# Performance work log

Hardware: AMD Instinct MI355X
Metric: run time of the kernel (lower is better)

The kernel has to match this reference:

```python
import jax, jax.numpy as jnp
import numpy as np

BN_EPS = 1e-5

def setup_inputs() -> dict:
    key = jax.random.key(0)
    ks = jax.random.split(key, 7)
    B, D, A = 16384, 768, 51
    s = 1.0 / np.sqrt(D)
    return {
        "x": jax.random.normal(ks[0], (B, D), dtype=jnp.float32),
        "W_embed": jax.random.uniform(ks[1], (D, D), minval=-s, maxval=s, dtype=jnp.float32),
        "b_embed": jax.random.uniform(ks[2], (D,), minval=-s, maxval=s, dtype=jnp.float32),
        "W_attr": jax.random.uniform(ks[3], (A, D), minval=-s, maxval=s, dtype=jnp.float32),  # stacked per-attribute (dim->1) heads
        "b_attr": jax.random.uniform(ks[4], (A,), minval=-s, maxval=s, dtype=jnp.float32),
        "gamma": jnp.ones((A,), dtype=jnp.float32),
        "beta": jnp.zeros((A,), dtype=jnp.float32),
    }

def reference(x, W_embed, b_embed, W_attr, b_attr, gamma, beta):
    # word_embed: Linear(dim, dim)
    h = x @ W_embed.T + b_embed                      # [B, D]
    # fused per-attribute heads: cat of attr_num (dim->1) linears == one (dim->attr_num) matmul
    logits = h @ W_attr.T + b_attr                    # [B, A]
    # BatchNorm1d (training mode: batch statistics, biased variance)
    mean = jnp.mean(logits, axis=0)
    var = jnp.var(logits, axis=0)
    y = (logits - mean) * jax.lax.rsqrt(var + BN_EPS) * gamma + beta
    return y
```

## Files before the change

kernel.cpp:

```cpp
#include <hip/hip_runtime.h>
#include <hip/hip_bf16.h>

typedef _Float16 halfx8 __attribute__((ext_vector_type(8)));
typedef _Float16 halfx4 __attribute__((ext_vector_type(4)));
typedef float floatx4 __attribute__((ext_vector_type(4)));

#define GLOBAL_AS __attribute__((address_space(1)))
#define LDS_AS __attribute__((address_space(3)))

__device__ __forceinline__ void async_copy_16(const _Float16* g, _Float16* l) {
    __builtin_amdgcn_global_load_lds((GLOBAL_AS void*)g, (LDS_AS void*)l, 16, 0, 0);
}

#define PM 16384
#define PD 768
#define PA 51
#define PA_PAD 64

__global__ void convert_x_kernel(const float* __restrict__ src, _Float16* __restrict__ dst) {
    int idx = blockIdx.x * 256 + threadIdx.x;
    float4 v = ((const float4*)src)[idx];
    halfx4 h;
    h[0] = (_Float16)v.x; h[1] = (_Float16)v.y; h[2] = (_Float16)v.z; h[3] = (_Float16)v.w;
    *(halfx4*)(dst + (size_t)idx * 4) = h;
}

__global__ void convert_w_kernel(const float* __restrict__ We, const float* __restrict__ Wa,
                                 _Float16* __restrict__ we16, _Float16* __restrict__ wa16,
                                 float* __restrict__ stats) {
    int b = blockIdx.x, t = threadIdx.x;
    if (b < 576) {
        int idx = b * 256 + t;
        float4 v = ((const float4*)We)[idx];
        halfx4 h;
        h[0] = (_Float16)v.x; h[1] = (_Float16)v.y; h[2] = (_Float16)v.z; h[3] = (_Float16)v.w;
        *(halfx4*)(we16 + (size_t)idx * 4) = h;
    } else if (b < 624) {
        int j = (b - 576) * 256 + t;
        halfx4 h;
        if (j < (PA * PD) / 4) {
            float4 v = ((const float4*)Wa)[j];
            h[0] = (_Float16)v.x; h[1] = (_Float16)v.y; h[2] = (_Float16)v.z; h[3] = (_Float16)v.w;
        } else {
            h[0] = (_Float16)0.f; h[1] = (_Float16)0.f; h[2] = (_Float16)0.f; h[3] = (_Float16)0.f;
        }
        *(halfx4*)(wa16 + (size_t)j * 4) = h;
    } else {
        if (t < 128) stats[t] = 0.f;
    }
}

__global__ __launch_bounds__(256) void gemm1_kernel(
    const _Float16* __restrict__ A,
    const _Float16* __restrict__ B,
    const float* __restrict__ bias,
    _Float16* __restrict__ H)
{
    __shared__ _Float16 As[128 * 64];
    __shared__ _Float16 Bs[128 * 64];
    const int tid = threadIdx.x;
    const int wave = tid >> 6;
    const int lane = tid & 63;
    const int quad = lane >> 4;
    const int l16 = lane & 15;
    const int wm = wave >> 1;
    const int wn = wave & 1;

    int b = blockIdx.x;
    int xcd = b & 7;
    int q = b >> 3;
    int mt = xcd * 16 + (q & 15);
    int nt = q >> 4;
    const int row0 = mt * 128;
    const int col0 = nt * 128;

    const int r_in = lane >> 3;
    const int koff = (lane & 7) * 8;

    const _Float16* Ag = A + (size_t)row0 * PD + koff;
    const _Float16* Bg = B + (size_t)col0 * PD + koff;

    floatx4 acc[4][4];
    #pragma unroll
    for (int i = 0; i < 4; ++i)
        #pragma unroll
        for (int j = 0; j < 4; ++j)
            acc[i][j] = (floatx4){0.f, 0.f, 0.f, 0.f};

    for (int kt = 0; kt < PD; kt += 64) {
        #pragma unroll
        for (int j = 0; j < 4; ++j) {
            int i = wave * 4 + j;
            async_copy_16(Ag + (size_t)(i * 8 + r_in) * PD + kt, &As[i * 512]);
            async_copy_16(Bg + (size_t)(i * 8 + r_in) * PD + kt, &Bs[i * 512]);
        }
        __syncthreads();
        #pragma unroll
        for (int ks = 0; ks < 2; ++ks) {
            halfx8 af[4], bf[4];
            #pragma unroll
            for (int mi = 0; mi < 4; ++mi)
                af[mi] = *(const halfx8*)&As[(wm * 64 + mi * 16 + l16) * 64 + ks * 32 + quad * 8];
            #pragma unroll
            for (int ni = 0; ni < 4; ++ni)
                bf[ni] = *(const halfx8*)&Bs[(wn * 64 + ni * 16 + l16) * 64 + ks * 32 + quad * 8];
            #pragma unroll
            for (int mi = 0; mi < 4; ++mi)
                #pragma unroll
                for (int ni = 0; ni < 4; ++ni)
                    acc[mi][ni] = __builtin_amdgcn_mfma_f32_16x16x32_f16(af[mi], bf[ni], acc[mi][ni], 0, 0, 0);
        }
        __syncthreads();
    }

    #pragma unroll
    for (int ni = 0; ni < 4; ++ni) {
        int col = col0 + wn * 64 + ni * 16 + l16;
        float bv = bias[col];
        #pragma unroll
        for (int mi = 0; mi < 4; ++mi) {
            int rowb = row0 + wm * 64 + mi * 16 + quad * 4;
            #pragma unroll
            for (int r = 0; r < 4; ++r)
                H[(size_t)(rowb + r) * PD + col] = (_Float16)(acc[mi][ni][r] + bv);
        }
    }
}

__global__ __launch_bounds__(256) void gemm2_kernel(
    const _Float16* __restrict__ Hm,
    const _Float16* __restrict__ Wa,
    const float* __restrict__ b_attr,
    float* __restrict__ logits,
    float* __restrict__ stats)
{
    __shared__ _Float16 As[128 * 64];
    __shared__ _Float16 Bs[64 * 64];
    __shared__ float s_sum[64];
    __shared__ float s_ssq[64];
    const int tid = threadIdx.x;
    const int wave = tid >> 6;
    const int lane = tid & 63;
    const int quad = lane >> 4;
    const int l16 = lane & 15;
    const int row0 = blockIdx.x * 128;
    const int r_in = lane >> 3;
    const int koff = (lane & 7) * 8;

    if (tid < 64) { s_sum[tid] = 0.f; s_ssq[tid] = 0.f; }

    const _Float16* Ag = Hm + (size_t)row0 * PD + koff;
    const _Float16* Bg = Wa + koff;

    floatx4 acc[2][4];
    #pragma unroll
    for (int i = 0; i < 2; ++i)
        #pragma unroll
        for (int j = 0; j < 4; ++j)
            acc[i][j] = (floatx4){0.f, 0.f, 0.f, 0.f};

    for (int kt = 0; kt < PD; kt += 64) {
        #pragma unroll
        for (int j = 0; j < 4; ++j) {
            int i = wave * 4 + j;
            async_copy_16(Ag + (size_t)(i * 8 + r_in) * PD + kt, &As[i * 512]);
        }
        #pragma unroll
        for (int j = 0; j < 2; ++j) {
            int i = wave * 2 + j;
            async_copy_16(Bg + (size_t)(i * 8 + r_in) * PD + kt, &Bs[i * 512]);
        }
        __syncthreads();
        #pragma unroll
        for (int ks = 0; ks < 2; ++ks) {
            halfx8 af[2], bf[4];
            #pragma unroll
            for (int mi = 0; mi < 2; ++mi)
                af[mi] = *(const halfx8*)&As[(wave * 32 + mi * 16 + l16) * 64 + ks * 32 + quad * 8];
            #pragma unroll
            for (int ni = 0; ni < 4; ++ni)
                bf[ni] = *(const halfx8*)&Bs[(ni * 16 + l16) * 64 + ks * 32 + quad * 8];
            #pragma unroll
            for (int mi = 0; mi < 2; ++mi)
                #pragma unroll
                for (int ni = 0; ni < 4; ++ni)
                    acc[mi][ni] = __builtin_amdgcn_mfma_f32_16x16x32_f16(af[mi], bf[ni], acc[mi][ni], 0, 0, 0);
        }
        __syncthreads();
    }

    #pragma unroll
    for (int ni = 0; ni < 4; ++ni) {
        int col = ni * 16 + l16;
        if (col < PA) {
            float bv = b_attr[col];
            float ps = 0.f, pss = 0.f;
            #pragma unroll
            for (int mi = 0; mi < 2; ++mi) {
                int rowb = row0 + wave * 32 + mi * 16 + quad * 4;
                #pragma unroll
                for (int r = 0; r < 4; ++r) {
                    float v = acc[mi][ni][r] + bv;
                    logits[(size_t)(rowb + r) * PA + col] = v;
                    ps += v; pss += v * v;
                }
            }
            atomicAdd(&s_sum[col], ps);
            atomicAdd(&s_ssq[col], pss);
        }
    }
    __syncthreads();
    if (tid < PA) {
        atomicAdd(&stats[tid], s_sum[tid]);
        atomicAdd(&stats[64 + tid], s_ssq[tid]);
    }
}

__global__ void bn_finalize_kernel(const float* __restrict__ logits,
                                   const float* __restrict__ stats,
                                   const float* __restrict__ gamma,
                                   const float* __restrict__ beta,
                                   float* __restrict__ out, int total) {
    __shared__ float s_scale[PA];
    __shared__ float s_shift[PA];
    int t = threadIdx.x;
    if (t < PA) {
        const float invB = 1.0f / (float)PM;
        float mean = stats[t] * invB;
        float var = stats[64 + t] * invB - mean * mean;
        float inv = rsqrtf(var + 1e-5f);
        float g = gamma[t] * inv;
        s_scale[t] = g;
        s_shift[t] = beta[t] - mean * g;
    }
    __syncthreads();
    int idx = blockIdx.x * 256 + t;
    if (idx < total) {
        int col = idx % PA;
        out[idx] = logits[idx] * s_scale[col] + s_shift[col];
    }
}

extern "C" void kernel_launch(void* const* d_in, const int* in_sizes, int n_in,
                              void* d_out, int out_size, void* d_ws, size_t ws_size,
                              hipStream_t stream) {
    const float* x       = (const float*)d_in[0];
    const float* W_embed = (const float*)d_in[1];
    const float* b_embed = (const float*)d_in[2];
    const float* W_attr  = (const float*)d_in[3];
    const float* b_attr  = (const float*)d_in[4];
    const float* gamma   = (const float*)d_in[5];
    const float* beta    = (const float*)d_in[6];
    float* out = (float*)d_out;

    char* ws = (char*)d_ws;
    _Float16* x_f16  = (_Float16*)(ws);
    _Float16* we16   = (_Float16*)(ws + 25165824);
    _Float16* wa16   = (_Float16*)(ws + 26345472);
    _Float16* h_f16  = (_Float16*)(ws + 26443776);
    float*    logits = (float*)   (ws + 51609600);
    float*    stats  = (float*)   (ws + 54951936);

    convert_x_kernel<<<12288, 256, 0, stream>>>(x, x_f16);
    convert_w_kernel<<<625, 256, 0, stream>>>(W_embed, W_attr, we16, wa16, stats);
    gemm1_kernel<<<768, 256, 0, stream>>>(x_f16, we16, b_embed, h_f16);
    gemm2_kernel<<<128, 256, 0, stream>>>(h_f16, wa16, b_attr, logits, stats);
    bn_finalize_kernel<<<3264, 256, 0, stream>>>(logits, stats, gamma, beta, out, PM * PA);
}
```

Before: 163.3 us.

## XOR-swizzle LDS layout, merge convert kernels, halve gemm2 row tile

Applies an XOR swizzle to the K-chunk index when staging A/B tiles into LDS in both GEMMs, so that the halfx8 fragment reads avoid LDS bank conflicts. Merges the x and weight fp16 conversion kernels into a single launch to save one kernel launch. Shrinks gemm2 tiles from 128 to 64 rows, doubling its grid to 256 blocks so more CUs are used, at the cost of more global stats atomics and less reuse of the Wa tile.

Result: faster. 153.3 us (-6.1%).

```diff
diff --git a/kernel.cpp b/kernel.cpp
--- a/kernel.cpp
+++ b/kernel.cpp
@@ -17,26 +17,26 @@
 #define PA 51
 #define PA_PAD 64
 
-__global__ void convert_x_kernel(const float* __restrict__ src, _Float16* __restrict__ dst) {
-    int idx = blockIdx.x * 256 + threadIdx.x;
-    float4 v = ((const float4*)src)[idx];
-    halfx4 h;
-    h[0] = (_Float16)v.x; h[1] = (_Float16)v.y; h[2] = (_Float16)v.z; h[3] = (_Float16)v.w;
-    *(halfx4*)(dst + (size_t)idx * 4) = h;
-}
-
-__global__ void convert_w_kernel(const float* __restrict__ We, const float* __restrict__ Wa,
-                                 _Float16* __restrict__ we16, _Float16* __restrict__ wa16,
-                                 float* __restrict__ stats) {
+
+__global__ void convert_all_kernel(const float* __restrict__ x, const float* __restrict__ We,
+                                   const float* __restrict__ Wa,
+                                   _Float16* __restrict__ x16, _Float16* __restrict__ we16,
+                                   _Float16* __restrict__ wa16, float* __restrict__ stats) {
     int b = blockIdx.x, t = threadIdx.x;
-    if (b < 576) {
+    if (b < 12288) {
         int idx = b * 256 + t;
+        float4 v = ((const float4*)x)[idx];
+        halfx4 h;
+        h[0] = (_Float16)v.x; h[1] = (_Float16)v.y; h[2] = (_Float16)v.z; h[3] = (_Float16)v.w;
+        *(halfx4*)(x16 + (size_t)idx * 4) = h;
+    } else if (b < 12288 + 576) {
+        int idx = (b - 12288) * 256 + t;
         float4 v = ((const float4*)We)[idx];
         halfx4 h;
         h[0] = (_Float16)v.x; h[1] = (_Float16)v.y; h[2] = (_Float16)v.z; h[3] = (_Float16)v.w;
         *(halfx4*)(we16 + (size_t)idx * 4) = h;
-    } else if (b < 624) {
-        int j = (b - 576) * 256 + t;
+    } else if (b < 12288 + 624) {
+        int j = (b - 12288 - 576) * 256 + t;
         halfx4 h;
         if (j < (PA * PD) / 4) {
             float4 v = ((const float4*)Wa)[j];
@@ -75,10 +75,10 @@
     const int col0 = nt * 128;
 
     const int r_in = lane >> 3;
-    const int koff = (lane & 7) * 8;
-
-    const _Float16* Ag = A + (size_t)row0 * PD + koff;
-    const _Float16* Bg = B + (size_t)col0 * PD + koff;
+    const int ksw = ((lane & 7) ^ r_in) * 8;
+
+    const _Float16* Ag = A + (size_t)row0 * PD + ksw;
+    const _Float16* Bg = B + (size_t)col0 * PD + ksw;
 
     floatx4 acc[4][4];
     #pragma unroll
@@ -100,10 +100,12 @@
             halfx8 af[4], bf[4];
             #pragma unroll
             for (int mi = 0; mi < 4; ++mi)
-                af[mi] = *(const halfx8*)&As[(wm * 64 + mi * 16 + l16) * 64 + ks * 32 + quad * 8];
+                af[mi] = *(const halfx8*)&As[(wm * 64 + mi * 16 + l16) * 64 +
+                                             (((ks * 4 + quad) ^ (l16 & 7)) << 3)];
             #pragma unroll
             for (int ni = 0; ni < 4; ++ni)
-                bf[ni] = *(const halfx8*)&Bs[(wn * 64 + ni * 16 + l16) * 64 + ks * 32 + quad * 8];
+                bf[ni] = *(const halfx8*)&Bs[(wn * 64 + ni * 16 + l16) * 64 +
+                                             (((ks * 4 + quad) ^ (l16 & 7)) << 3)];
             #pragma unroll
             for (int mi = 0; mi < 4; ++mi)
                 #pragma unroll
@@ -134,7 +136,7 @@
     float* __restrict__ logits,
     float* __restrict__ stats)
 {
-    __shared__ _Float16 As[128 * 64];
+    __shared__ _Float16 As[64 * 64];
     __shared__ _Float16 Bs[64 * 64];
     __shared__ float s_sum[64];
     __shared__ float s_ssq[64];
@@ -143,26 +145,24 @@
     const int lane = tid & 63;
     const int quad = lane >> 4;
     const int l16 = lane & 15;
-    const int row0 = blockIdx.x * 128;
+    const int row0 = blockIdx.x * 64;
     const int r_in = lane >> 3;
-    const int koff = (lane & 7) * 8;
+    const int ksw = ((lane & 7) ^ r_in) * 8;
 
     if (tid < 64) { s_sum[tid] = 0.f; s_ssq[tid] = 0.f; }
 
-    const _Float16* Ag = Hm + (size_t)row0 * PD + koff;
-    const _Float16* Bg = Wa + koff;
-
-    floatx4 acc[2][4];
-    #pragma unroll
-    for (int i = 0; i < 2; ++i)
-        #pragma unroll
-        for (int j = 0; j < 4; ++j)
-            acc[i][j] = (floatx4){0.f, 0.f, 0.f, 0.f};
+    const _Float16* Ag = Hm + (size_t)row0 * PD + ksw;
+    const _Float16* Bg = Wa + ksw;
+
+    floatx4 acc[4];
+    #pragma unroll
+    for (int j = 0; j < 4; ++j)
+        acc[j] = (floatx4){0.f, 0.f, 0.f, 0.f};
 
     for (int kt = 0; kt < PD; kt += 64) {
         #pragma unroll
-        for (int j = 0; j < 4; ++j) {
-            int i = wave * 4 + j;
+        for (int j = 0; j < 2; ++j) {
+            int i = wave * 2 + j;
             async_copy_16(Ag + (size_t)(i * 8 + r_in) * PD + kt, &As[i * 512]);
         }
         #pragma unroll
@@ -173,18 +173,16 @@
         __syncthreads();
         #pragma unroll
         for (int ks = 0; ks < 2; ++ks) {
-            halfx8 af[2], bf[4];
-            #pragma unroll
-            for (int mi = 0; mi < 2; ++mi)
-                af[mi] = *(const halfx8*)&As[(wave * 32 + mi * 16 + l16) * 64 + ks * 32 + quad * 8];
+            halfx8 af, bf[4];
+            af = *(const halfx8*)&As[(wave * 16 + l16) * 64 +
+                                     (((ks * 4 + quad) ^ (l16 & 7)) << 3)];
             #pragma unroll
             for (int ni = 0; ni < 4; ++ni)
-                bf[ni] = *(const halfx8*)&Bs[(ni * 16 + l16) * 64 + ks * 32 + quad * 8];
-            #pragma unroll
-            for (int mi = 0; mi < 2; ++mi)
-                #pragma unroll
-                for (int ni = 0; ni < 4; ++ni)
-                    acc[mi][ni] = __builtin_amdgcn_mfma_f32_16x16x32_f16(af[mi], bf[ni], acc[mi][ni], 0, 0, 0);
+                bf[ni] = *(const halfx8*)&Bs[(ni * 16 + l16) * 64 +
+                                             (((ks * 4 + quad) ^ (l16 & 7)) << 3)];
+            #pragma unroll
+            for (int ni = 0; ni < 4; ++ni)
+                acc[ni] = __builtin_amdgcn_mfma_f32_16x16x32_f16(af, bf[ni], acc[ni], 0, 0, 0);
         }
         __syncthreads();
     }
@@ -195,15 +193,12 @@
         if (col < PA) {
             float bv = b_attr[col];
             float ps = 0.f, pss = 0.f;
-            #pragma unroll
-            for (int mi = 0; mi < 2; ++mi) {
-                int rowb = row0 + wave * 32 + mi * 16 + quad * 4;
-                #pragma unroll
-                for (int r = 0; r < 4; ++r) {
-                    float v = acc[mi][ni][r] + bv;
-                    logits[(size_t)(rowb + r) * PA + col] = v;
-                    ps += v; pss += v * v;
-                }
+            int rowb = row0 + wave * 16 + quad * 4;
+            #pragma unroll
+            for (int r = 0; r < 4; ++r) {
+                float v = acc[ni][r] + bv;
+                logits[(size_t)(rowb + r) * PA + col] = v;
+                ps += v; pss += v * v;
             }
             atomicAdd(&s_sum[col], ps);
             atomicAdd(&s_ssq[col], pss);
@@ -261,9 +256,8 @@
     float*    logits = (float*)   (ws + 51609600);
     float*    stats  = (float*)   (ws + 54951936);
 
-    convert_x_kernel<<<12288, 256, 0, stream>>>(x, x_f16);
-    convert_w_kernel<<<625, 256, 0, stream>>>(W_embed, W_attr, we16, wa16, stats);
+    convert_all_kernel<<<12913, 256, 0, stream>>>(x, W_embed, W_attr, x_f16, we16, wa16, stats);
     gemm1_kernel<<<768, 256, 0, stream>>>(x_f16, we16, b_embed, h_f16);
-    gemm2_kernel<<<128, 256, 0, stream>>>(h_f16, wa16, b_attr, logits, stats);
+    gemm2_kernel<<<256, 256, 0, stream>>>(h_f16, wa16, b_attr, logits, stats);
     bn_finalize_kernel<<<3264, 256, 0, stream>>>(logits, stats, gamma, beta, out, PM * PA);
 }
```
